# Performance work log

Measured on AMD Instinct MI355X. Metric: run time of the kernel, lower is better.

Reference implementation:

```python
import jax, jax.numpy as jnp
import numpy as np

B, L, V, D = 8, 1024, 64, 64  # num_vars == d_model required by the module's g*h broadcast
EPS = 1e-5


def _layer_norm(x, gamma, beta):
    mu = jnp.mean(x, axis=-1, keepdims=True)
    var = jnp.mean(jnp.square(x - mu), axis=-1, keepdims=True)
    return (x - mu) * jax.lax.rsqrt(var + EPS) * gamma + beta


def setup_inputs() -> dict:
    key = jax.random.key(0)
    ks = jax.random.split(key, 20)
    s = 0.05
    inp = {
        'x': jax.random.normal(ks[0], (B, L, V), jnp.float32),
        # per-variable GRN(1, D, D) params, batched over V
        'W1': jax.random.normal(ks[1], (V, D), jnp.float32) * s,   # lin1 weight [in=1 -> D]
        'b1': jax.random.normal(ks[2], (V, D), jnp.float32) * s,
        'W2': jax.random.normal(ks[3], (V, D, D), jnp.float32) * s,
        'b2': jax.random.normal(ks[4], (V, D), jnp.float32) * s,
        'Wg': jax.random.normal(ks[5], (V, D, D), jnp.float32) * s,
        'bg': jax.random.normal(ks[6], (V, D), jnp.float32) * s,
        'Wsk': jax.random.normal(ks[7], (V, D), jnp.float32) * s,  # skip Linear(1, D)
        'bsk': jax.random.normal(ks[8], (V, D), jnp.float32) * s,
        'gamma': jnp.ones((V, D), jnp.float32),
        'beta': jnp.zeros((V, D), jnp.float32),
        # weight_net GRN(V*D, D, V) params
        'Wn1': jax.random.normal(ks[9], (V * D, D), jnp.float32) * s,
        'bn1': jax.random.normal(ks[10], (D,), jnp.float32) * s,
        'Wn2': jax.random.normal(ks[11], (D, D), jnp.float32) * s,
        'bn2': jax.random.normal(ks[12], (D,), jnp.float32) * s,
        'Wng': jax.random.normal(ks[13], (D, V), jnp.float32) * s,
        'bng': jax.random.normal(ks[14], (V,), jnp.float32) * s,
        'Wns': jax.random.normal(ks[15], (V * D, V), jnp.float32) * s,
        'bns': jax.random.normal(ks[16], (V,), jnp.float32) * s,
        'ngamma': jnp.ones((V,), jnp.float32),
        'nbeta': jnp.zeros((V,), jnp.float32),
    }
    return inp


def reference(x, W1, b1, W2, b2, Wg, bg, Wsk, bsk, gamma, beta,
              Wn1, bn1, Wn2, bn2, Wng, bng, Wns, bns, ngamma, nbeta):
    Bx, Lx, Vx = x.shape
    # --- per-variable GRN(1, D, D), batched over the variable axis ---
    h1 = jax.nn.elu(x[..., None] * W1 + b1)                      # [B,L,V,D]
    h2 = jnp.einsum('blvd,vde->blve', h1, W2) + b2               # [B,L,V,D]
    g = jax.nn.sigmoid(jnp.einsum('blvd,vde->blve', h2, Wg) + bg)
    skip = x[..., None] * Wsk + bsk                              # [B,L,V,D]
    stacked = _layer_norm(skip + g * h2, gamma, beta)            # [B,L,V,D]
    # --- weight net GRN(V*D, D, V) + softmax (note: requires V == D) ---
    flat = stacked.reshape(Bx, Lx, Vx * stacked.shape[-1])
    hw = jax.nn.elu(flat @ Wn1 + bn1)                            # [B,L,D]
    hw = hw @ Wn2 + bn2                                          # [B,L,D]
    gw = jax.nn.sigmoid(hw @ Wng + bng)                          # [B,L,V]
    skw = flat @ Wns + bns                                       # [B,L,V]
    weights = jax.nn.softmax(_layer_norm(skw + gw * hw, ngamma, nbeta), axis=-1)
    return jnp.einsum('blv,blvd->bld', weights, stacked)
```

## Files before the change

kernel.cpp:

```cpp
#include <hip/hip_runtime.h>
#include <hip/hip_bf16.h>
#include <math.h>

#define NV 64
#define ND 64
#define NTOK 8192
#define LN_EPS 1e-5f
#define KSPLIT 8
#define KRANGE (4096 / KSPLIT)

typedef __attribute__((ext_vector_type(8))) short s8v;
typedef __attribute__((ext_vector_type(4))) float f4v;
typedef __attribute__((ext_vector_type(4))) int   i4v;

__device__ __forceinline__ float sigm_f(float x) { return 1.f / (1.f + __expf(-x)); }
__device__ __forceinline__ float elu_f(float x)  { return x > 0.f ? x : (__expf(x) - 1.f); }

__device__ __forceinline__ float bf16_to_f(unsigned short s) {
    union { unsigned int u; float f; } c; c.u = ((unsigned int)s) << 16;
    return c.f;
}
__device__ __forceinline__ unsigned short bf16_rn(float f) {
    union { float f; unsigned int u; } c; c.f = f;
    return (unsigned short)((c.u + 0x8000u) >> 16);
}

__global__ __launch_bounds__(256) void vsn_prepack(
    const float* __restrict__ W2, const float* __restrict__ Wg,
    const float* __restrict__ Wn1, const float* __restrict__ Wns,
    short* __restrict__ w2b, short* __restrict__ wgb,
    __hip_bfloat16* __restrict__ wct)
{
    __shared__ float T[64][65];
    const int b = blockIdx.x, t = threadIdx.x;

    if (b < 64) {
        const float* src = W2 + (size_t)b * 4096;
        short* dst = w2b + (size_t)b * 4096;
        #pragma unroll
        for (int pass = 0; pass < 2; ++pass) {
            #pragma unroll
            for (int i = 0; i < 16; ++i) {
                int id = i * 256 + t;
                T[id & 63][id >> 6] = src[id];
            }
            __syncthreads();
            #pragma unroll
            for (int i = 0; i < 16; ++i) {
                int id = i * 256 + t;
                dst[id] = (short)bf16_rn(T[id >> 6][id & 63]);
            }
            __syncthreads();
            src = Wg + (size_t)b * 4096;
            dst = wgb + (size_t)b * 4096;
        }
    } else {
        int tb = b - 64;
        int half = tb >> 6, kt = tb & 63;
        const float* src = (half == 0 ? Wn1 : Wns) + (size_t)(kt * 64) * 64;
        #pragma unroll
        for (int i = 0; i < 16; ++i) {
            int id = i * 256 + t;
            T[id & 63][id >> 6] = src[id];
        }
        __syncthreads();
        #pragma unroll
        for (int i = 0; i < 16; ++i) {
            int id = i * 256 + t;
            int n = id >> 6, r = id & 63;
            wct[(size_t)(half * 64 + n) * 4096 + kt * 64 + r] =
                __float2bfloat16(T[n][r]);
        }
    }
}

__global__ __launch_bounds__(256) void vsn_stage1(
    const float* __restrict__ x,
    const float* __restrict__ W1, const float* __restrict__ b1,
    const short* __restrict__ w2b, const short* __restrict__ wgb,
    const float* __restrict__ b2, const float* __restrict__ bg,
    const float* __restrict__ Wsk, const float* __restrict__ bsk,
    const float* __restrict__ gamma, const float* __restrict__ beta,
    __hip_bfloat16* __restrict__ stb)
{
    const int t = threadIdx.x;
    const int wave = t >> 6, lane = t & 63;
    const int m16 = lane & 15, quad = lane >> 4;
    const int tile0 = blockIdx.x * 32;
    const int v = blockIdx.y * 4 + wave;

    __shared__ float xs[4][32];
    __shared__ __align__(16) unsigned short h2s[4][32][72];

    if (lane < 32) xs[wave][lane] = x[(size_t)(tile0 + lane) * NV + v];

    s8v a[2][2];
    #pragma unroll
    for (int kt = 0; kt < 2; ++kt) {
        float w1k[8], b1k[8];
        *(float4*)&w1k[0] = *(const float4*)(W1 + v * 64 + kt * 32 + quad * 8);
        *(float4*)&w1k[4] = *(const float4*)(W1 + v * 64 + kt * 32 + quad * 8 + 4);
        *(float4*)&b1k[0] = *(const float4*)(b1 + v * 64 + kt * 32 + quad * 8);
        *(float4*)&b1k[4] = *(const float4*)(b1 + v * 64 + kt * 32 + quad * 8 + 4);
        #pragma unroll
        for (int mi = 0; mi < 2; ++mi) {
            float xv = xs[wave][mi * 16 + m16];
            float h[8];
            #pragma unroll
            for (int j = 0; j < 8; ++j) h[j] = elu_f(fmaf(xv, w1k[j], b1k[j]));
            i4v av;
            #pragma unroll
            for (int p = 0; p < 4; ++p) {
                unsigned int u0 = __float_as_uint(h[2 * p]);
                unsigned int u1 = __float_as_uint(h[2 * p + 1]);
                av[p] = (int)((u1 & 0xffff0000u) | (u0 >> 16));
            }
            a[mi][kt] = *(s8v*)&av;
        }
    }

    f4v hacc[2][4];
    #pragma unroll
    for (int mi = 0; mi < 2; ++mi)
        #pragma unroll
        for (int ni = 0; ni < 4; ++ni) hacc[mi][ni] = (f4v){0.f, 0.f, 0.f, 0.f};

    const size_t wb = (size_t)v * 4096;
    #pragma unroll
    for (int ni = 0; ni < 4; ++ni)
        #pragma unroll
        for (int kt = 0; kt < 2; ++kt) {
            s8v bh = *(const s8v*)(w2b + wb + (size_t)(ni * 16 + m16) * 64 + kt * 32 + quad * 8);
            #pragma unroll
            for (int mi = 0; mi < 2; ++mi)
                hacc[mi][ni] = __builtin_amdgcn_mfma_f32_16x16x32_bf16(a[mi][kt], bh, hacc[mi][ni], 0, 0, 0);
        }
    {
        float b2d[4];
        #pragma unroll
        for (int ni = 0; ni < 4; ++ni) b2d[ni] = b2[v * 64 + ni * 16 + m16];
        #pragma unroll
        for (int mi = 0; mi < 2; ++mi)
            #pragma unroll
            for (int ni = 0; ni < 4; ++ni)
                #pragma unroll
                for (int r = 0; r < 4; ++r) hacc[mi][ni][r] += b2d[ni];
    }

    #pragma unroll
    for (int mi = 0; mi < 2; ++mi)
        #pragma unroll
        for (int ni = 0; ni < 4; ++ni)
            #pragma unroll
            for (int r = 0; r < 4; ++r)
                h2s[wave][mi * 16 + quad * 4 + r][ni * 16 + m16] =
                    (unsigned short)(__float_as_uint(hacc[mi][ni][r]) >> 16);

    s8v c[2][2];
    #pragma unroll
    for (int mi = 0; mi < 2; ++mi)
        #pragma unroll
        for (int kt = 0; kt < 2; ++kt)
            c[mi][kt] = *(const s8v*)&h2s[wave][mi * 16 + m16][kt * 32 + quad * 8];

    f4v gacc[2][4];
    #pragma unroll
    for (int mi = 0; mi < 2; ++mi)
        #pragma unroll
        for (int ni = 0; ni < 4; ++ni) gacc[mi][ni] = (f4v){0.f, 0.f, 0.f, 0.f};
    #pragma unroll
    for (int ni = 0; ni < 4; ++ni)
        #pragma unroll
        for (int kt = 0; kt < 2; ++kt) {
            s8v bh = *(const s8v*)(wgb + wb + (size_t)(ni * 16 + m16) * 64 + kt * 32 + quad * 8);
            #pragma unroll
            for (int mi = 0; mi < 2; ++mi)
                gacc[mi][ni] = __builtin_amdgcn_mfma_f32_16x16x32_bf16(c[mi][kt], bh, gacc[mi][ni], 0, 0, 0);
        }

    {
        float bgd[4], wskd[4], bskd[4];
        #pragma unroll
        for (int ni = 0; ni < 4; ++ni) {
            int d = v * 64 + ni * 16 + m16;
            bgd[ni] = bg[d]; wskd[ni] = Wsk[d]; bskd[ni] = bsk[d];
        }
        float xtok[2][4];
        #pragma unroll
        for (int mi = 0; mi < 2; ++mi)
            #pragma unroll
            for (int r = 0; r < 4; ++r) xtok[mi][r] = xs[wave][mi * 16 + quad * 4 + r];
        #pragma unroll
        for (int mi = 0; mi < 2; ++mi)
            #pragma unroll
            for (int ni = 0; ni < 4; ++ni)
                #pragma unroll
                for (int r = 0; r < 4; ++r) {
                    float g = sigm_f(gacc[mi][ni][r] + bgd[ni]);
                    gacc[mi][ni][r] = fmaf(xtok[mi][r], wskd[ni], bskd[ni]) + g * hacc[mi][ni][r];
                }
    }

    {
        float gamd[4], betd[4];
        #pragma unroll
        for (int ni = 0; ni < 4; ++ni) {
            int d = v * 64 + ni * 16 + m16;
            gamd[ni] = gamma[d]; betd[ni] = beta[d];
        }
        #pragma unroll
        for (int mi = 0; mi < 2; ++mi)
            #pragma unroll
            for (int r = 0; r < 4; ++r) {
                float s0 = gacc[mi][0][r], s1 = gacc[mi][1][r], s2 = gacc[mi][2][r], s3 = gacc[mi][3][r];
                float sum = s0 + s1 + s2 + s3;
                float sq  = s0 * s0 + s1 * s1 + s2 * s2 + s3 * s3;
                #pragma unroll
                for (int m = 1; m < 16; m <<= 1) { sum += __shfl_xor(sum, m); sq += __shfl_xor(sq, m); }
                float mu  = sum * 0.015625f;
                float var = sq * 0.015625f - mu * mu;
                float rs  = rsqrtf(var + LN_EPS);
                size_t base = (size_t)(tile0 + mi * 16 + quad * 4 + r) * 4096 + (size_t)v * 64 + m16;
                #pragma unroll
                for (int ni = 0; ni < 4; ++ni)
                    stb[base + ni * 16] = __hip_bfloat16_raw{
                        bf16_rn((gacc[mi][ni][r] - mu) * rs * gamd[ni] + betd[ni])};
            }
    }
}

__global__ __launch_bounds__(512) void vsn_stage2a(
    const __hip_bfloat16* __restrict__ stb,
    const __hip_bfloat16* __restrict__ wct,
    float* __restrict__ part)
{
    const int t = threadIdx.x;
    const int wave = t >> 6, lane = t & 63;
    const int mtile = wave >> 2;
    const int n0 = (wave & 3) * 32;
    const int tok0 = blockIdx.x * 128 + mtile * 64;
    const int s = blockIdx.y;
    const int k0 = s * KRANGE;
    const int m16 = lane & 15, quad = lane >> 4;

    const short* A  = (const short*)stb;
    const short* Bw = (const short*)wct;

    f4v acc[4][2];
    #pragma unroll
    for (int i = 0; i < 4; ++i)
        #pragma unroll
        for (int j = 0; j < 2; ++j)
            acc[i][j] = (f4v){0.f, 0.f, 0.f, 0.f};

    const short* arow = A  + (size_t)(tok0 + m16) * 4096 + quad * 8;
    const short* brow = Bw + (size_t)(n0 + m16) * 4096 + quad * 8;

    s8v abuf[3][4], bbuf[3][2];
    #pragma unroll
    for (int st = 0; st < 2; ++st) {
        int k = k0 + st * 32;
        #pragma unroll
        for (int i = 0; i < 4; ++i)
            abuf[st][i] = *(const s8v*)(arow + (size_t)i * 16 * 4096 + k);
        #pragma unroll
        for (int j = 0; j < 2; ++j)
            bbuf[st][j] = *(const s8v*)(brow + (size_t)j * 16 * 4096 + k);
    }

    #pragma unroll
    for (int it = 0; it < 16; ++it) {
        if (it < 14) {
            const int st = (it + 2) % 3;
            const int k = k0 + (it + 2) * 32;
            #pragma unroll
            for (int i = 0; i < 4; ++i)
                abuf[st][i] = *(const s8v*)(arow + (size_t)i * 16 * 4096 + k);
            #pragma unroll
            for (int j = 0; j < 2; ++j)
                bbuf[st][j] = *(const s8v*)(brow + (size_t)j * 16 * 4096 + k);
        }
        const int cs = it % 3;
        #pragma unroll
        for (int i = 0; i < 4; ++i)
            #pragma unroll
            for (int j = 0; j < 2; ++j)
                acc[i][j] = __builtin_amdgcn_mfma_f32_16x16x32_bf16(
                    abuf[cs][i], bbuf[cs][j], acc[i][j], 0, 0, 0);
    }

    #pragma unroll
    for (int i = 0; i < 4; ++i)
        #pragma unroll
        for (int j = 0; j < 2; ++j)
            #pragma unroll
            for (int r = 0; r < 4; ++r)
                part[((size_t)(tok0 + i * 16 + quad * 4 + r)) * (KSPLIT * 128)
                     + s * 128 + n0 + j * 16 + m16] = acc[i][j][r];
}

__global__ __launch_bounds__(256) void vsn_stage2b(
    const __hip_bfloat16* __restrict__ stb, const float* __restrict__ part,
    const float* __restrict__ bn1,
    const float* __restrict__ Wn2, const float* __restrict__ bn2,
    const float* __restrict__ Wng, const float* __restrict__ bng,
    const float* __restrict__ bns,
    const float* __restrict__ ngamma, const float* __restrict__ nbeta,
    float* __restrict__ out)
{
    const int t = threadIdx.x;
    const int tok0 = blockIdx.x * 8;
    const int lane = t & 63, wv = t >> 6;

    __shared__ __align__(16) float hw1_s[8][64];
    __shared__ __align__(16) float skw_s[8][64];
    __shared__ __align__(16) float hw2_s[8][64];
    __shared__ float s2_s[8][64];
    __shared__ float w_s[8][64];

    #pragma unroll
    for (int tk = 0; tk < 2; ++tk) {
        int tl = wv * 2 + tk;
        const float* pr = part + (size_t)(tok0 + tl) * (KSPLIT * 128)
                        + (lane >> 5) * 128 + (lane & 31) * 4;
        float4 a0 = *(const float4*)(pr);
        float4 a1 = *(const float4*)(pr + 256);
        float4 a2 = *(const float4*)(pr + 512);
        float4 a3 = *(const float4*)(pr + 768);
        float tv[4];
        tv[0] = a0.x + a1.x + a2.x + a3.x;
        tv[1] = a0.y + a1.y + a2.y + a3.y;
        tv[2] = a0.z + a1.z + a2.z + a3.z;
        tv[3] = a0.w + a1.w + a2.w + a3.w;
        #pragma unroll
        for (int c = 0; c < 4; ++c) tv[c] += __shfl_xor(tv[c], 32);
        if (lane < 16) {
            int j0 = lane * 4;
            float4 bb = *(const float4*)(bn1 + j0);
            hw1_s[tl][j0 + 0] = elu_f(tv[0] + bb.x);
            hw1_s[tl][j0 + 1] = elu_f(tv[1] + bb.y);
            hw1_s[tl][j0 + 2] = elu_f(tv[2] + bb.z);
            hw1_s[tl][j0 + 3] = elu_f(tv[3] + bb.w);
        } else if (lane < 32) {
            int j0 = (lane - 16) * 4;
            float4 bb = *(const float4*)(bns + j0);
            skw_s[tl][j0 + 0] = tv[0] + bb.x;
            skw_s[tl][j0 + 1] = tv[1] + bb.y;
            skw_s[tl][j0 + 2] = tv[2] + bb.z;
            skw_s[tl][j0 + 3] = tv[3] + bb.w;
        }
    }
    __syncthreads();

    #pragma unroll
    for (int i = 0; i < 2; ++i) {
        int oidx = i * 256 + t;
        int tt = oidx >> 6, jj = oidx & 63;
        float acc = bn2[jj];
        #pragma unroll
        for (int k4 = 0; k4 < 16; ++k4) {
            float4 h = *(const float4*)&hw1_s[tt][k4 * 4];
            acc += h.x * Wn2[(k4*4+0)*64+jj] + h.y * Wn2[(k4*4+1)*64+jj]
                 + h.z * Wn2[(k4*4+2)*64+jj] + h.w * Wn2[(k4*4+3)*64+jj];
        }
        hw2_s[tt][jj] = acc;
    }
    __syncthreads();

    #pragma unroll
    for (int i = 0; i < 2; ++i) {
        int oidx = i * 256 + t;
        int tt = oidx >> 6, vv = oidx & 63;
        float acc = bng[vv];
        #pragma unroll
        for (int k4 = 0; k4 < 16; ++k4) {
            float4 h = *(const float4*)&hw2_s[tt][k4 * 4];
            acc += h.x * Wng[(k4*4+0)*64+vv] + h.y * Wng[(k4*4+1)*64+vv]
                 + h.z * Wng[(k4*4+2)*64+vv] + h.w * Wng[(k4*4+3)*64+vv];
        }
        float gw = sigm_f(acc);
        s2_s[tt][vv] = skw_s[tt][vv] + gw * hw2_s[tt][vv];
    }
    __syncthreads();

    const int vloc = lane >> 3, d8 = (lane & 7) * 8;
    s8v r0[8], r1[8];
    {
        const short* s0 = (const short*)stb + (size_t)(tok0 + wv * 2) * 4096 + d8;
        const short* s1 = s0 + 4096;
        #pragma unroll
        for (int vc = 0; vc < 8; ++vc) {
            r0[vc] = *(const s8v*)(s0 + (vc * 8 + vloc) * 64);
            r1[vc] = *(const s8v*)(s1 + (vc * 8 + vloc) * 64);
        }
    }

    if (t < 128) {
        int tt = t >> 4, l = t & 15;
        float z[4]; float sum = 0.f, sq = 0.f;
        #pragma unroll
        for (int i = 0; i < 4; ++i) { z[i] = s2_s[tt][l + 16 * i]; sum += z[i]; sq += z[i] * z[i]; }
        #pragma unroll
        for (int m = 1; m < 16; m <<= 1) { sum += __shfl_xor(sum, m); sq += __shfl_xor(sq, m); }
        float mu  = sum * 0.015625f;
        float var = sq * 0.015625f - mu * mu;
        float rs  = rsqrtf(var + LN_EPS);
        float ln[4]; float mx = -1e30f;
        #pragma unroll
        for (int i = 0; i < 4; ++i) {
            ln[i] = (z[i] - mu) * rs * ngamma[l + 16 * i] + nbeta[l + 16 * i];
            mx = fmaxf(mx, ln[i]);
        }
        #pragma unroll
        for (int m = 1; m < 16; m <<= 1) mx = fmaxf(mx, __shfl_xor(mx, m));
        float es = 0.f; float ev[4];
        #pragma unroll
        for (int i = 0; i < 4; ++i) { ev[i] = __expf(ln[i] - mx); es += ev[i]; }
        #pragma unroll
        for (int m = 1; m < 16; m <<= 1) es += __shfl_xor(es, m);
        float inv = 1.f / es;
        #pragma unroll
        for (int i = 0; i < 4; ++i) w_s[tt][l + 16 * i] = ev[i] * inv;
    }
    __syncthreads();

    {
        float acc0[8], acc1[8];
        #pragma unroll
        for (int j = 0; j < 8; ++j) { acc0[j] = 0.f; acc1[j] = 0.f; }
        #pragma unroll
        for (int vc = 0; vc < 8; ++vc) {
            int v = vc * 8 + vloc;
            float w0 = w_s[wv * 2][v], w1 = w_s[wv * 2 + 1][v];
            #pragma unroll
            for (int j = 0; j < 8; ++j) {
                acc0[j] = fmaf(w0, bf16_to_f((unsigned short)r0[vc][j]), acc0[j]);
                acc1[j] = fmaf(w1, bf16_to_f((unsigned short)r1[vc][j]), acc1[j]);
            }
        }
        #pragma unroll
        for (int m = 8; m <= 32; m <<= 1)
            #pragma unroll
            for (int j = 0; j < 8; ++j) {
                acc0[j] += __shfl_xor(acc0[j], m);
                acc1[j] += __shfl_xor(acc1[j], m);
            }
        if (lane < 8) {
            float* op = out + (size_t)(tok0 + wv * 2) * 64 + lane * 8;
            *(float4*)op       = make_float4(acc0[0], acc0[1], acc0[2], acc0[3]);
            *(float4*)(op + 4) = make_float4(acc0[4], acc0[5], acc0[6], acc0[7]);
            op += 64;
            *(float4*)op       = make_float4(acc1[0], acc1[1], acc1[2], acc1[3]);
            *(float4*)(op + 4) = make_float4(acc1[4], acc1[5], acc1[6], acc1[7]);
        }
    }
}

extern "C" void kernel_launch(void* const* d_in, const int* in_sizes, int n_in,
                              void* d_out, int out_size, void* d_ws, size_t ws_size,
                              hipStream_t stream) {
    const float* x     = (const float*)d_in[0];
    const float* W1    = (const float*)d_in[1];
    const float* b1    = (const float*)d_in[2];
    const float* W2    = (const float*)d_in[3];
    const float* b2    = (const float*)d_in[4];
    const float* Wg    = (const float*)d_in[5];
    const float* bg    = (const float*)d_in[6];
    const float* Wsk   = (const float*)d_in[7];
    const float* bsk   = (const float*)d_in[8];
    const float* gamma = (const float*)d_in[9];
    const float* beta  = (const float*)d_in[10];
    const float* Wn1   = (const float*)d_in[11];
    const float* bn1   = (const float*)d_in[12];
    const float* Wn2   = (const float*)d_in[13];
    const float* bn2   = (const float*)d_in[14];
    const float* Wng   = (const float*)d_in[15];
    const float* bng   = (const float*)d_in[16];
    const float* Wns   = (const float*)d_in[17];
    const float* bns   = (const float*)d_in[18];
    const float* ngam  = (const float*)d_in[19];
    const float* nbet  = (const float*)d_in[20];

    char* ws = (char*)d_ws;
    __hip_bfloat16* stb = (__hip_bfloat16*)ws;
    __hip_bfloat16* wct = (__hip_bfloat16*)(ws + (64u << 20));
    float* part = (float*)(ws + (65u << 20));
    short* w2b = (short*)(ws + (97u << 20));
    short* wgb = w2b + 262144;
    float* outp = (float*)d_out;

    vsn_prepack<<<dim3(192), 256, 0, stream>>>(W2, Wg, Wn1, Wns, w2b, wgb, wct);
    vsn_stage1<<<dim3(NTOK / 32, 16), 256, 0, stream>>>(
        x, W1, b1, w2b, wgb, b2, bg, Wsk, bsk, gamma, beta, stb);
    vsn_stage2a<<<dim3(NTOK / 128, KSPLIT), 512, 0, stream>>>(stb, wct, part);
    vsn_stage2b<<<dim3(NTOK / 8), 256, 0, stream>>>(
        stb, part, bn1, Wn2, bn2, Wng, bng, bns, ngam, nbet, outp);
}
```

Before: 227.3 us.

## Fuse weight-net first GEMM into stage1 via per-variable-group partial sums

Removes the separate split-K GEMM kernel that re-read the bf16 stacked activations. Each stage1 block now multiplies its freshly normalized tile, staged in shared memory, by the matching K-slice of the packed Wn1/Wns weights using MFMA. The four waves' partials are reduced in shared memory and written as one of 16 partial slices, which stage2b then sums. The trade-off is a larger partial buffer (16 slices instead of 8) and extra shared memory and register pressure in stage1, in exchange for skipping a full re-read of the activation tensor and one kernel launch.

```diff
diff --git a/kernel.cpp b/kernel.cpp
--- a/kernel.cpp
+++ b/kernel.cpp
@@ -6,8 +6,7 @@
 #define ND 64
 #define NTOK 8192
 #define LN_EPS 1e-5f
-#define KSPLIT 8
-#define KRANGE (4096 / KSPLIT)
+#define NSLICE 16
 
 typedef __attribute__((ext_vector_type(8))) short s8v;
 typedef __attribute__((ext_vector_type(4))) float f4v;
@@ -81,16 +80,20 @@
     const float* __restrict__ b2, const float* __restrict__ bg,
     const float* __restrict__ Wsk, const float* __restrict__ bsk,
     const float* __restrict__ gamma, const float* __restrict__ beta,
-    __hip_bfloat16* __restrict__ stb)
+    const __hip_bfloat16* __restrict__ wct,
+    __hip_bfloat16* __restrict__ stb,
+    float* __restrict__ part)
 {
     const int t = threadIdx.x;
     const int wave = t >> 6, lane = t & 63;
     const int m16 = lane & 15, quad = lane >> 4;
     const int tile0 = blockIdx.x * 32;
-    const int v = blockIdx.y * 4 + wave;
+    const int vg = blockIdx.y;
+    const int v = vg * 4 + wave;
 
     __shared__ float xs[4][32];
     __shared__ __align__(16) unsigned short h2s[4][32][72];
+    __shared__ __align__(16) float P2[32][132];
 
     if (lane < 32) xs[wave][lane] = x[(size_t)(tile0 + lane) * NV + v];
 
@@ -201,6 +204,7 @@
                 }
     }
 
+    unsigned short* stw = &h2s[wave][0][0];
     {
         float gamd[4], betd[4];
         #pragma unroll
@@ -220,83 +224,78 @@
                 float mu  = sum * 0.015625f;
                 float var = sq * 0.015625f - mu * mu;
                 float rs  = rsqrtf(var + LN_EPS);
-                size_t base = (size_t)(tile0 + mi * 16 + quad * 4 + r) * 4096 + (size_t)v * 64 + m16;
-                #pragma unroll
-                for (int ni = 0; ni < 4; ++ni)
-                    stb[base + ni * 16] = __hip_bfloat16_raw{
-                        bf16_rn((gacc[mi][ni][r] - mu) * rs * gamd[ni] + betd[ni])};
-            }
-    }
-}
-
-__global__ __launch_bounds__(512) void vsn_stage2a(
-    const __hip_bfloat16* __restrict__ stb,
-    const __hip_bfloat16* __restrict__ wct,
-    float* __restrict__ part)
-{
-    const int t = threadIdx.x;
-    const int wave = t >> 6, lane = t & 63;
-    const int mtile = wave >> 2;
-    const int n0 = (wave & 3) * 32;
-    const int tok0 = blockIdx.x * 128 + mtile * 64;
-    const int s = blockIdx.y;
-    const int k0 = s * KRANGE;
-    const int m16 = lane & 15, quad = lane >> 4;
-
-    const short* A  = (const short*)stb;
-    const short* Bw = (const short*)wct;
-
-    f4v acc[4][2];
-    #pragma unroll
-    for (int i = 0; i < 4; ++i)
-        #pragma unroll
-        for (int j = 0; j < 2; ++j)
-            acc[i][j] = (f4v){0.f, 0.f, 0.f, 0.f};
-
-    const short* arow = A  + (size_t)(tok0 + m16) * 4096 + quad * 8;
-    const short* brow = Bw + (size_t)(n0 + m16) * 4096 + quad * 8;
-
-    s8v abuf[3][4], bbuf[3][2];
-    #pragma unroll
-    for (int st = 0; st < 2; ++st) {
-        int k = k0 + st * 32;
-        #pragma unroll
-        for (int i = 0; i < 4; ++i)
-            abuf[st][i] = *(const s8v*)(arow + (size_t)i * 16 * 4096 + k);
-        #pragma unroll
-        for (int j = 0; j < 2; ++j)
-            bbuf[st][j] = *(const s8v*)(brow + (size_t)j * 16 * 4096 + k);
-    }
-
-    #pragma unroll
-    for (int it = 0; it < 16; ++it) {
-        if (it < 14) {
-            const int st = (it + 2) % 3;
-            const int k = k0 + (it + 2) * 32;
-            #pragma unroll
-            for (int i = 0; i < 4; ++i)
-                abuf[st][i] = *(const s8v*)(arow + (size_t)i * 16 * 4096 + k);
-            #pragma unroll
-            for (int j = 0; j < 2; ++j)
-                bbuf[st][j] = *(const s8v*)(brow + (size_t)j * 16 * 4096 + k);
-        }
-        const int cs = it % 3;
-        #pragma unroll
-        for (int i = 0; i < 4; ++i)
-            #pragma unroll
-            for (int j = 0; j < 2; ++j)
-                acc[i][j] = __builtin_amdgcn_mfma_f32_16x16x32_bf16(
-                    abuf[cs][i], bbuf[cs][j], acc[i][j], 0, 0, 0);
-    }
-
-    #pragma unroll
-    for (int i = 0; i < 4; ++i)
-        #pragma unroll
-        for (int j = 0; j < 2; ++j)
-            #pragma unroll
-            for (int r = 0; r < 4; ++r)
-                part[((size_t)(tok0 + i * 16 + quad * 4 + r)) * (KSPLIT * 128)
-                     + s * 128 + n0 + j * 16 + m16] = acc[i][j][r];
+                int row = mi * 16 + quad * 4 + r;
+                size_t base = (size_t)(tile0 + row) * 4096 + (size_t)v * 64 + m16;
+                #pragma unroll
+                for (int ni = 0; ni < 4; ++ni) {
+                    unsigned short q = bf16_rn((gacc[mi][ni][r] - mu) * rs * gamd[ni] + betd[ni]);
+                    stb[base + ni * 16] = __hip_bfloat16_raw{q};
+                    stw[row * 72 + ni * 16 + m16] = q;
+                }
+            }
+    }
+
+    s8v af[2][2];
+    #pragma unroll
+    for (int mi = 0; mi < 2; ++mi)
+        #pragma unroll
+        for (int kt = 0; kt < 2; ++kt)
+            af[mi][kt] = *(const s8v*)&stw[(mi * 16 + m16) * 72 + kt * 32 + quad * 8];
+
+    f4v pacc[2][8];
+    #pragma unroll
+    for (int mi = 0; mi < 2; ++mi)
+        #pragma unroll
+        for (int ng = 0; ng < 8; ++ng) pacc[mi][ng] = (f4v){0.f, 0.f, 0.f, 0.f};
+
+    {
+        const short* wr = (const short*)wct;
+        #pragma unroll
+        for (int kt = 0; kt < 2; ++kt)
+            #pragma unroll
+            for (int ng = 0; ng < 8; ++ng) {
+                s8v bfr = *(const s8v*)(wr + (size_t)(ng * 16 + m16) * 4096
+                                        + v * 64 + kt * 32 + quad * 8);
+                pacc[0][ng] = __builtin_amdgcn_mfma_f32_16x16x32_bf16(af[0][kt], bfr, pacc[0][ng], 0, 0, 0);
+                pacc[1][ng] = __builtin_amdgcn_mfma_f32_16x16x32_bf16(af[1][kt], bfr, pacc[1][ng], 0, 0, 0);
+            }
+    }
+
+    float* P1 = (float*)&h2s[0][0][0];
+    __syncthreads();
+    if ((wave & 1) == 0) {
+        float* P = (wave == 0) ? P1 : &P2[0][0];
+        #pragma unroll
+        for (int mi = 0; mi < 2; ++mi)
+            #pragma unroll
+            for (int ng = 0; ng < 8; ++ng)
+                #pragma unroll
+                for (int r = 0; r < 4; ++r)
+                    P[(mi * 16 + quad * 4 + r) * 132 + ng * 16 + m16] = pacc[mi][ng][r];
+    }
+    __syncthreads();
+    if ((wave & 1) == 1) {
+        float* P = (wave == 1) ? P1 : &P2[0][0];
+        #pragma unroll
+        for (int mi = 0; mi < 2; ++mi)
+            #pragma unroll
+            for (int ng = 0; ng < 8; ++ng)
+                #pragma unroll
+                for (int r = 0; r < 4; ++r)
+                    P[(mi * 16 + quad * 4 + r) * 132 + ng * 16 + m16] += pacc[mi][ng][r];
+    }
+    __syncthreads();
+    {
+        int m = t >> 3, nc = (t & 7) * 16;
+        float* dst = part + (size_t)(tile0 + m) * (NSLICE * 128) + (size_t)vg * 128 + nc;
+        #pragma unroll
+        for (int q = 0; q < 4; ++q) {
+            float4 p1 = *(float4*)&P1[m * 132 + nc + q * 4];
+            float4 p2 = *(float4*)&P2[m][nc + q * 4];
+            *(float4*)(dst + q * 4) = make_float4(p1.x + p2.x, p1.y + p2.y,
+                                                  p1.z + p2.z, p1.w + p2.w);
+        }
+    }
 }
 
 __global__ __launch_bounds__(256) void vsn_stage2b(
@@ -321,17 +320,14 @@
     #pragma unroll
     for (int tk = 0; tk < 2; ++tk) {
         int tl = wv * 2 + tk;
-        const float* pr = part + (size_t)(tok0 + tl) * (KSPLIT * 128)
+        const float* pr = part + (size_t)(tok0 + tl) * (NSLICE * 128)
                         + (lane >> 5) * 128 + (lane & 31) * 4;
-        float4 a0 = *(const float4*)(pr);
-        float4 a1 = *(const float4*)(pr + 256);
-        float4 a2 = *(const float4*)(pr + 512);
-        float4 a3 = *(const float4*)(pr + 768);
-        float tv[4];
-        tv[0] = a0.x + a1.x + a2.x + a3.x;
-        tv[1] = a0.y + a1.y + a2.y + a3.y;
-        tv[2] = a0.z + a1.z + a2.z + a3.z;
-        tv[3] = a0.w + a1.w + a2.w + a3.w;
+        float tv[4] = {0.f, 0.f, 0.f, 0.f};
+        #pragma unroll
+        for (int i = 0; i < 8; ++i) {
+            float4 a = *(const float4*)(pr + i * 256);
+            tv[0] += a.x; tv[1] += a.y; tv[2] += a.z; tv[3] += a.w;
+        }
         #pragma unroll
         for (int c = 0; c < 4; ++c) tv[c] += __shfl_xor(tv[c], 32);
         if (lane < 16) {
@@ -485,14 +481,13 @@
     __hip_bfloat16* stb = (__hip_bfloat16*)ws;
     __hip_bfloat16* wct = (__hip_bfloat16*)(ws + (64u << 20));
     float* part = (float*)(ws + (65u << 20));
-    short* w2b = (short*)(ws + (97u << 20));
+    short* w2b = (short*)(ws + (129u << 20));
     short* wgb = w2b + 262144;
     float* outp = (float*)d_out;
 
     vsn_prepack<<<dim3(192), 256, 0, stream>>>(W2, Wg, Wn1, Wns, w2b, wgb, wct);
     vsn_stage1<<<dim3(NTOK / 32, 16), 256, 0, stream>>>(
-        x, W1, b1, w2b, wgb, b2, bg, Wsk, bsk, gamma, beta, stb);
-    vsn_stage2a<<<dim3(NTOK / 128, KSPLIT), 512, 0, stream>>>(stb, wct, part);
+        x, W1, b1, w2b, wgb, b2, bg, Wsk, bsk, gamma, beta, wct, stb, part);
     vsn_stage2b<<<dim3(NTOK / 8), 256, 0, stream>>>(
         stb, part, bn1, Wn2, bn2, Wng, bng, bns, ngam, nbet, outp);
 }
```

Result: slower. 232.3 us (+2.2%).
